# Kernel tuning notes

Hardware: AMD Instinct MI355X
Metric: run time of the kernel (lower is better)

## Reference

```python
import jax, jax.numpy as jnp
import numpy as np

BATCH, SEQ_LEN, ENC_IN = 64, 1536, 7
D_MODEL, N_HEADS, D_FF, E_LAYERS = 256, 8, 1024, 2
K_MA, FACTOR = 25, 1
EPS = 1e-5


def setup_inputs() -> dict:
    key = jax.random.key(0)
    ks = jax.random.split(key, 16)
    s = 0.02
    f32 = jnp.float32
    inp = {
        "x_enc": jax.random.normal(ks[0], (BATCH, SEQ_LEN, ENC_IN), f32),
        "emb_w": jax.random.normal(ks[1], (D_MODEL, ENC_IN, 3), f32) * s,
        "Wq": jax.random.normal(ks[2], (E_LAYERS, D_MODEL, D_MODEL), f32) * s,
        "bq": jnp.zeros((E_LAYERS, D_MODEL), f32),
        "Wk": jax.random.normal(ks[3], (E_LAYERS, D_MODEL, D_MODEL), f32) * s,
        "bk": jnp.zeros((E_LAYERS, D_MODEL), f32),
        "Wv": jax.random.normal(ks[4], (E_LAYERS, D_MODEL, D_MODEL), f32) * s,
        "bv": jnp.zeros((E_LAYERS, D_MODEL), f32),
        "Wo": jax.random.normal(ks[5], (E_LAYERS, D_MODEL, D_MODEL), f32) * s,
        "bo": jnp.zeros((E_LAYERS, D_MODEL), f32),
        "Wc1": jax.random.normal(ks[6], (E_LAYERS, D_FF, D_MODEL), f32) * s,
        "bc1": jnp.zeros((E_LAYERS, D_FF), f32),
        "Wc2": jax.random.normal(ks[7], (E_LAYERS, D_MODEL, D_FF), f32) * s,
        "bc2": jnp.zeros((E_LAYERS, D_MODEL), f32),
        "ln_w": jnp.ones((D_MODEL,), f32),
        "ln_b": jnp.zeros((D_MODEL,), f32),
        "proj_w": jax.random.normal(ks[8], (176, 2 * D_MODEL), f32) * s,
        "proj_b": jnp.zeros((176,), f32),
    }
    return inp


def _moving_avg(x, k):
    # x: [B,L,D]; replicate-pad (k-1)//2 both ends, mean filter size k (stride 1)
    p = (k - 1) // 2
    xp = jnp.concatenate([jnp.repeat(x[:, :1], p, axis=1), x,
                          jnp.repeat(x[:, -1:], p, axis=1)], axis=1)
    cs = jnp.cumsum(xp, axis=1)
    cs = jnp.concatenate([jnp.zeros_like(cs[:, :1]), cs], axis=1)
    return (cs[:, k:] - cs[:, :-k]) / k


def _decomp(x):
    mm = _moving_avg(x, K_MA)
    return x - mm, mm


def _autocorrelation(q, k, v):
    # q,k,v: [B,L,H,E] -> [B,L,H,E]
    B, L, H, E = q.shape
    qf = jnp.fft.rfft(jnp.transpose(q, (0, 2, 3, 1)), axis=-1)
    kf = jnp.fft.rfft(jnp.transpose(k, (0, 2, 3, 1)), axis=-1)
    corr = jnp.fft.irfft(qf * jnp.conj(kf), n=L, axis=-1)   # [B,H,E,L]
    vals = jnp.transpose(v, (0, 2, 3, 1))                    # [B,H,E,L]
    top_k = int(FACTOR * np.log(L))
    mean_corr = corr.mean(axis=(1, 2))                       # [B,L]
    weights, delay = jax.lax.top_k(mean_corr, top_k)         # [B,top_k]
    tmp_corr = jax.nn.softmax(weights, axis=-1)
    idx0 = jnp.arange(L)
    agg = jnp.zeros_like(vals)
    for i in range(top_k):                                    # small fixed count (7)
        idx = (idx0[None, :] + delay[:, i, None]) % L         # [B,L] circular delay
        pat = jnp.take_along_axis(vals, jnp.broadcast_to(idx[:, None, None, :], vals.shape), axis=-1)
        agg = agg + pat * tmp_corr[:, i, None, None, None]
    return jnp.transpose(agg, (0, 3, 1, 2))


def _attn_layer(x, Wq, bq, Wk, bk, Wv, bv, Wo, bo):
    B, L, _ = x.shape
    E = D_MODEL // N_HEADS
    q = (x @ Wq.T + bq).reshape(B, L, N_HEADS, E)
    k = (x @ Wk.T + bk).reshape(B, L, N_HEADS, E)
    v = (x @ Wv.T + bv).reshape(B, L, N_HEADS, E)
    out = _autocorrelation(q, k, v).reshape(B, L, D_MODEL)
    return out @ Wo.T + bo


def reference(x_enc, emb_w, Wq, bq, Wk, bk, Wv, bv, Wo, bo, Wc1, bc1, Wc2, bc2, ln_w, ln_b, proj_w, proj_b):
    # token embedding: circular-padded Conv1d(enc_in -> d_model, kernel 3, no bias)
    xp = jnp.concatenate([x_enc[:, -1:], x_enc, x_enc[:, :1]], axis=1)
    x = (jnp.einsum('blc,dc->bld', xp[:, :-2], emb_w[:, :, 0])
         + jnp.einsum('blc,dc->bld', xp[:, 1:-1], emb_w[:, :, 1])
         + jnp.einsum('blc,dc->bld', xp[:, 2:], emb_w[:, :, 2]))
    for l in range(E_LAYERS):
        a = _attn_layer(x, Wq[l], bq[l], Wk[l], bk[l], Wv[l], bv[l], Wo[l], bo[l])
        x, _ = _decomp(x + a)
        y = jax.nn.gelu(jnp.einsum('bld,fd->blf', x, Wc1[l]) + bc1[l], approximate=False)
        y = jnp.einsum('blf,df->bld', y, Wc2[l]) + bc2[l]
        x, _ = _decomp(x + y)
    # my_Layernorm: LN then subtract seq-mean
    mu = x.mean(-1, keepdims=True)
    var = ((x - mu) ** 2).mean(-1, keepdims=True)
    xh = (x - mu) / jnp.sqrt(var + EPS) * ln_w + ln_b
    x = xh - xh.mean(axis=1, keepdims=True)
    out = jnp.concatenate([x.mean(axis=1), x.max(axis=1)], axis=-1)  # [B, 2*d_model]
    out = jax.nn.gelu(out, approximate=False)
    return out @ proj_w.T + proj_b
```

## Files before the change

kernel.cpp:

```cpp
#include <hip/hip_runtime.h>
#include <math.h>

typedef _Float16 half_t;
typedef _Float16 half4 __attribute__((ext_vector_type(4)));
typedef _Float16 half8 __attribute__((ext_vector_type(8)));
typedef short short8 __attribute__((ext_vector_type(8)));
typedef float f32x4 __attribute__((ext_vector_type(4)));
typedef unsigned short u16;
typedef unsigned short u16x4 __attribute__((ext_vector_type(4)));

#define L_SEQ 1536

__device__ __forceinline__ u16 f2bf(float f){
  unsigned u = __float_as_uint(f);
  return (u16)((u + 0x7FFFu + ((u>>16)&1u)) >> 16);
}
__device__ __forceinline__ float bf2f(u16 h){ return __uint_as_float(((unsigned)h)<<16); }
__device__ __forceinline__ float gelu_f(float x){ return 0.5f*x*(1.f+erff(x*0.70710678118f)); }

__device__ __forceinline__ void load_lds16(const void* g, void* l){
  __builtin_amdgcn_global_load_lds((const __attribute__((address_space(1))) void*)g,
                                   (__attribute__((address_space(3))) void*)l, 16, 0, 0);
}
__device__ __forceinline__ f32x4 mfma_bf(short8 a, short8 b, f32x4 c){
  return __builtin_amdgcn_mfma_f32_16x16x32_bf16(a,b,c,0,0,0);
}
__device__ __forceinline__ f32x4 mfma_fp(half8 a, half8 b, f32x4 c){
  return __builtin_amdgcn_mfma_f32_16x16x32_f16(a,b,c,0,0,0);
}

__device__ __forceinline__ void store_pair(float v, size_t row, int d, u16* X2B){
  size_t r2 = row*512 + d;
  u16 hi = f2bf(v);
  X2B[r2] = hi;
  X2B[r2+256] = f2bf(v - bf2f(hi));
}

__global__ __launch_bounds__(256) void w4b_k(const float* __restrict__ W, u16* __restrict__ W4, int n){
  int i = blockIdx.x*256 + threadIdx.x;
  if (i >= n) return;
  int ro = i >> 8, c = i & 255;
  float v = W[i];
  u16 hi = f2bf(v);
  u16 lo = f2bf(v - bf2f(hi));
  u16* r = W4 + (size_t)ro*1024;
  r[c] = hi; r[c+256] = hi; r[c+512] = lo; r[c+768] = lo;
}
__global__ __launch_bounds__(256) void castb_k(const float* __restrict__ W, u16* __restrict__ Wb, int n){
  for (int i = blockIdx.x*256 + threadIdx.x; i < n; i += gridDim.x*256)
    Wb[i] = f2bf(W[i]);
}

__global__ __launch_bounds__(256) void embed_k(const float* __restrict__ XE, const float* __restrict__ EW,
                                               u16* __restrict__ X2B){
  __shared__ float xs[66*7];
  int b = blockIdx.x / 24, lc = blockIdx.x % 24;
  int l0 = lc*64;
  int tid = threadIdx.x;
  for (int i = tid; i < 66*7; i += 256){
    int r = i/7, c = i%7;
    int g = l0 - 1 + r; if (g < 0) g += L_SEQ; if (g >= L_SEQ) g -= L_SEQ;
    xs[i] = XE[((size_t)b*L_SEQ + g)*7 + c];
  }
  __syncthreads();
  int d = tid;
  float wp[21];
  #pragma unroll
  for (int i=0;i<21;i++) wp[i] = EW[d*21+i];
  for (int j = 0; j < 64; j++){
    float acc = 0.f;
    #pragma unroll
    for (int c = 0; c < 7; c++)
      #pragma unroll
      for (int k = 0; k < 3; k++) acc += xs[(j+k)*7+c] * wp[c*3+k];
    store_pair(acc, (size_t)b*L_SEQ + l0 + j, d, X2B);
  }
}

template<int EPI, bool KMOD>
__global__ __launch_bounds__(256) void gemm_k(const u16* __restrict__ A, int lda,
                                              const u16* __restrict__ B, int ldb,
                                              const float* __restrict__ bias,
                                              void* __restrict__ C, int ldc,
                                              const u16* __restrict__ res,
                                              int K){
  __shared__ __align__(16) u16 As[128*32];
  __shared__ __align__(16) u16 Bs[128*32];
  const int tid = threadIdx.x;
  const int wv = tid>>6, ln = tid&63;
  const int lrow = ln&15, lk = ln>>4;
  const int bm = blockIdx.x, bn = blockIdx.y;
  const int wr = wv>>1, wc = wv&1;
  f32x4 acc[4][4];
  #pragma unroll
  for (int i=0;i<4;i++)
    #pragma unroll
    for (int j=0;j<4;j++) acc[i][j] = f32x4{0.f,0.f,0.f,0.f};

  for (int k0 = 0; k0 < K; k0 += 32){
    int ka = KMOD ? (k0 & 511) : k0;
    #pragma unroll
    for (int p=0;p<2;p++){
      int chunk = (wv*2+p)*64 + ln;
      int row = chunk>>2, c16 = chunk&3;
      load_lds16(A + (size_t)(bm*128 + row)*lda + (ka + c16*8), &As[(size_t)chunk*8]);
      load_lds16(B + (size_t)(bn*128 + row)*ldb + (k0 + c16*8), &Bs[(size_t)chunk*8]);
    }
    __syncthreads();
    short8 av[4], bv[4];
    #pragma unroll
    for (int mi=0;mi<4;mi++) av[mi] = *(const short8*)&As[(wr*64 + mi*16 + lrow)*32 + lk*8];
    #pragma unroll
    for (int ni=0;ni<4;ni++) bv[ni] = *(const short8*)&Bs[(wc*64 + ni*16 + lrow)*32 + lk*8];
    #pragma unroll
    for (int mi=0;mi<4;mi++)
      #pragma unroll
      for (int ni=0;ni<4;ni++)
        acc[mi][ni] = mfma_bf(av[mi], bv[ni], acc[mi][ni]);
    __syncthreads();
  }

  #pragma unroll
  for (int mi=0;mi<4;mi++){
    #pragma unroll
    for (int ni=0;ni<4;ni++){
      int col = bn*128 + wc*64 + ni*16 + lrow;
      float bs = bias[col];
      #pragma unroll
      for (int r=0;r<4;r++){
        int row = bm*128 + wr*64 + mi*16 + lk*4 + r;
        float v = acc[mi][ni][r] + bs;
        if (EPI==0){ ((u16*)C)[(size_t)row*ldc + col] = f2bf(v); }
        else if (EPI==1){ ((u16*)C)[(size_t)row*ldc + col] = f2bf(gelu_f(v)); }
        else if (EPI==2){
          float rv = bf2f(res[(size_t)row*512 + col]) + bf2f(res[(size_t)row*512 + 256 + col]);
          ((float*)C)[(size_t)row*ldc + col] = v + rv;
        } else {
          half_t hi = (half_t)v;
          ((half_t*)C)[(size_t)row*512 + col] = hi;
          ((half_t*)C)[(size_t)row*512 + 256 + col] = (half_t)((v - (float)hi)*512.f);
        }
      }
    }
  }
}

__global__ __launch_bounds__(256) void gram_k(const u16* __restrict__ Q2, const u16* __restrict__ K2,
                                              float* __restrict__ MC){
  __shared__ __align__(16) union UN {
    struct { u16 As[256*32]; u16 Bs[64*32]; } s;
    float C[64][65];
  } u;
  const int tid = threadIdx.x, wv = tid>>6, ln = tid&63;
  const int lrow = ln&15, lk = ln>>4;
  int id = blockIdx.x;
  int low = id & 7, hi = id >> 3;
  int tb = hi & 7;
  int b  = ((hi >> 3) << 3) | low;
  const size_t base = (size_t)b*L_SEQ*512;
  f32x4 acc[4][4];
  #pragma unroll
  for (int i=0;i<4;i++)
    #pragma unroll
    for (int j=0;j<4;j++) acc[i][j] = f32x4{0.f,0.f,0.f,0.f};

  for (int jt = 0; jt < 24; jt++){
    int t0 = tb*192 + jt*64;
    for (int dt = 0; dt < 8; dt++){
      int d0 = dt*32;
      #pragma unroll
      for (int p=0;p<4;p++){
        int chunk = (p*4+wv)*64 + ln;
        int row = chunk>>2, c16 = chunk&3;
        int g = t0 + row; if (g >= L_SEQ) g -= L_SEQ;
        load_lds16(Q2 + base + (size_t)g*512 + d0 + c16*8, &u.s.As[(size_t)chunk*8]);
      }
      { int chunk = wv*64 + ln;
        int row = chunk>>2, c16 = chunk&3;
        load_lds16(K2 + base + (size_t)(jt*64+row)*512 + d0 + c16*8, &u.s.Bs[(size_t)chunk*8]); }
      __syncthreads();
      half8 av[4], bv[4];
      #pragma unroll
      for (int mi=0;mi<4;mi++) av[mi] = *(const half8*)&u.s.As[(wv*64 + mi*16 + lrow)*32 + lk*8];
      #pragma unroll
      for (int ni=0;ni<4;ni++) bv[ni] = *(const half8*)&u.s.Bs[(ni*16 + lrow)*32 + lk*8];
      #pragma unroll
      for (int mi=0;mi<4;mi++)
        #pragma unroll
        for (int ni=0;ni<4;ni++)
          acc[mi][ni] = mfma_fp(av[mi], bv[ni], acc[mi][ni]);
      __syncthreads();
    }
  }
  float dsum = 0.f;
  for (int r = 0; r < 4; r++){
    if (wv == r){
      #pragma unroll
      for (int mi=0;mi<4;mi++)
        #pragma unroll
        for (int ni=0;ni<4;ni++)
          #pragma unroll
          for (int rr=0;rr<4;rr++)
            u.C[mi*16 + lk*4 + rr][ni*16 + lrow] = acc[mi][ni][rr];
    }
    __syncthreads();
    if (tid < 192){
      int jlo = r*64 - tid;      if (jlo < 0) jlo = 0;
      int jhi = r*64 + 64 - tid; if (jhi > 64) jhi = 64;
      for (int j = jlo; j < jhi; j++) dsum += u.C[tid + j - r*64][j];
    }
    __syncthreads();
  }
  if (tid < 192) MC[(size_t)b*L_SEQ + tb*192 + tid] = dsum * (1.f/256.f);
}

__global__ __launch_bounds__(256) void topk_k(const float* __restrict__ MC, int* __restrict__ CANDI,
                                              int* __restrict__ NCAND){
  __shared__ float v[1536];
  __shared__ float rv[256]; __shared__ int ri[256];
  __shared__ float sred[256];
  __shared__ float s_margin;
  __shared__ float topv[16]; __shared__ int topi[16];
  int b = blockIdx.x, tid = threadIdx.x;
  const float* row = MC + (size_t)b*L_SEQ;
  float s = 0.f, ss = 0.f;
  for (int j=0;j<6;j++){ float x = row[tid+256*j]; v[tid+256*j] = x; s += x; ss += x*x; }
  sred[tid]=s; __syncthreads();
  for (int o=128;o>0;o>>=1){ if (tid<o) sred[tid]+=sred[tid+o]; __syncthreads(); }
  float mean = sred[0]*(1.f/1536.f); __syncthreads();
  sred[tid]=ss; __syncthreads();
  for (int o=128;o>0;o>>=1){ if (tid<o) sred[tid]+=sred[tid+o]; __syncthreads(); }
  if (tid==0){
    float var = sred[0]*(1.f/1536.f) - mean*mean; if (var < 0.f) var = 0.f;
    s_margin = 0.02f*sqrtf(var) + 1e-8f;
  }
  __syncthreads();
  for (int it = 0; it < 16; it++){
    float bv_ = -3.4e38f; int bi_ = 1<<30;
    for (int j=0;j<6;j++){ int idx = tid+256*j; float x = v[idx];
      if (x > bv_ || (x == bv_ && idx < bi_)){ bv_ = x; bi_ = idx; } }
    rv[tid]=bv_; ri[tid]=bi_; __syncthreads();
    for (int o=128;o>0;o>>=1){
      if (tid<o){
        float xo = rv[tid+o]; int io = ri[tid+o];
        if (xo > rv[tid] || (xo == rv[tid] && io < ri[tid])){ rv[tid]=xo; ri[tid]=io; }
      }
      __syncthreads();
    }
    if (tid==0){ topv[it]=rv[0]; topi[it]=ri[0]; v[ri[0]] = -3.4e38f; }
    __syncthreads();
  }
  if (tid==0){
    float thr = topv[6] - s_margin;
    int nc = 7; while (nc < 16 && topv[nc] >= thr) nc++;
    NCAND[b] = nc;
    for (int i=0;i<16;i++) CANDI[b*16+i] = topi[i];
  }
}

__global__ __launch_bounds__(256) void recompute3_k(const u16* __restrict__ Q2, const u16* __restrict__ K2,
                                                    const int* __restrict__ CANDI, const int* __restrict__ NCAND,
                                                    float* __restrict__ CANDV){
  int id = blockIdx.x;
  int low = id & 7, hi = id >> 3;
  int ci = hi & 15;
  int b = (hi >> 4)*8 + low;
  if (ci >= NCAND[b]) return;
  int tau = CANDI[b*16+ci];
  const half_t* qb = (const half_t*)Q2 + (size_t)b*L_SEQ*512;
  const half_t* kb = (const half_t*)K2 + (size_t)b*L_SEQ*512;
  int tid = threadIdx.x, wv = tid>>6, ln = tid&63;
  int d0 = ln*4;
  float acc = 0.f;
  #pragma unroll 4
  for (int t = wv; t < L_SEQ; t += 4){
    int g = t + tau; if (g >= L_SEQ) g -= L_SEQ;
    half4 qh = *(const half4*)(qb + (size_t)g*512 + d0);
    half4 ql = *(const half4*)(qb + (size_t)g*512 + 256 + d0);
    half4 kh = *(const half4*)(kb + (size_t)t*512 + d0);
    half4 kl = *(const half4*)(kb + (size_t)t*512 + 256 + d0);
    #pragma unroll
    for (int j=0;j<4;j++){
      float qv = (float)qh[j] + (float)ql[j]*(1.f/512.f);
      float kv = (float)kh[j] + (float)kl[j]*(1.f/512.f);
      acc += qv*kv;
    }
  }
  #pragma unroll
  for (int o=32;o>0;o>>=1) acc += __shfl_xor(acc,o);
  __shared__ float w4[4];
  if (ln==0) w4[wv]=acc;
  __syncthreads();
  if (tid==0) CANDV[b*16+ci] = (w4[0]+w4[1]+w4[2]+w4[3])*(1.f/256.f);
}

__global__ void select7_k(const int* __restrict__ CANDI, const float* __restrict__ CANDV,
                          const int* __restrict__ NCAND, int* __restrict__ DLY, float* __restrict__ WGT){
  int b = blockIdx.x;
  if (threadIdx.x != 0) return;
  int nc = NCAND[b];
  float vals[16]; int idx[16];
  #pragma unroll
  for (int i=0;i<16;i++){ vals[i] = (i<nc)? CANDV[b*16+i] : -3.4e38f; idx[i] = CANDI[b*16+i]; }
  for (int i=0;i<7;i++){
    int best=i;
    for (int j=i+1;j<16;j++)
      if (vals[j]>vals[best] || (vals[j]==vals[best] && idx[j]<idx[best])) best=j;
    float tv=vals[i]; vals[i]=vals[best]; vals[best]=tv;
    int ti=idx[i]; idx[i]=idx[best]; idx[best]=ti;
  }
  float m=vals[0], e[7], sum=0.f;
  #pragma unroll
  for (int i=0;i<7;i++){ e[i]=expf(vals[i]-m); sum+=e[i]; }
  #pragma unroll
  for (int i=0;i<7;i++){ WGT[b*8+i]=e[i]/sum; DLY[b*8+i]=idx[i]; }
}

__global__ __launch_bounds__(256) void agg_k(const u16* __restrict__ V, const int* __restrict__ DLY,
                                             const float* __restrict__ WGT, u16* __restrict__ AGG){
  int gid = blockIdx.x*256 + threadIdx.x;
  int b = gid / 49152;
  int rem = gid % 49152;
  int t = rem >> 5, du = rem & 31;
  float w[7]; int dl[7];
  #pragma unroll
  for (int i=0;i<7;i++){ w[i]=WGT[b*8+i]; dl[i]=DLY[b*8+i]; }
  float a[8] = {0,0,0,0,0,0,0,0};
  #pragma unroll
  for (int i=0;i<7;i++){
    int g = t + dl[i]; if (g >= L_SEQ) g -= L_SEQ;
    short8 hv = *(const short8*)(V + ((size_t)b*L_SEQ + g)*256 + du*8);
    #pragma unroll
    for (int j=0;j<8;j++) a[j] += w[i]*bf2f((u16)hv[j]);
  }
  short8 o;
  #pragma unroll
  for (int j=0;j<8;j++) o[j] = (short)f2bf(a[j]);
  *(short8*)(AGG + ((size_t)b*L_SEQ + t)*256 + du*8) = o;
}

__global__ __launch_bounds__(256) void decomp_k(const float* __restrict__ S, u16* __restrict__ X2B){
  int b = blockIdx.y, lc = blockIdx.x, d = threadIdx.x;
  const float* s = S + (size_t)b*L_SEQ*256;
  int l0 = lc*128;
  float w = 0.f;
  for (int j=-12;j<=12;j++){
    int g = l0+j; if (g < 0) g = 0; if (g > L_SEQ-1) g = L_SEQ-1;
    w += s[(size_t)g*256+d];
  }
  for (int l = l0; l < l0+128; l++){
    float c = s[(size_t)l*256+d];
    store_pair(c - w*(1.f/25.f), (size_t)b*L_SEQ + l, d, X2B);
    int ga = l+13; if (ga > L_SEQ-1) ga = L_SEQ-1;
    int gb = l-12; if (gb < 0) gb = 0;
    w += s[(size_t)ga*256+d] - s[(size_t)gb*256+d];
  }
}

__global__ __launch_bounds__(256) void ln_k(const u16* __restrict__ X2B, const float* __restrict__ LW,
                                            const float* __restrict__ LB, float* __restrict__ XH){
  int tid = threadIdx.x, wv = tid>>6, l_ = tid&63;
  f32x4 lw = *(const f32x4*)(LW + l_*4);
  f32x4 lb = *(const f32x4*)(LB + l_*4);
  size_t tok0 = (size_t)blockIdx.x*32 + wv*8;
  for (int it = 0; it < 8; it++){
    size_t tok = tok0 + it;
    const u16* xr = X2B + tok*512 + l_*4;
    u16x4 hi = *(const u16x4*)xr;
    u16x4 lo = *(const u16x4*)(xr+256);
    float v[4]; float s=0.f, ss=0.f;
    #pragma unroll
    for (int j=0;j<4;j++){ v[j] = bf2f(hi[j]) + bf2f(lo[j]); s += v[j]; ss += v[j]*v[j]; }
    #pragma unroll
    for (int o=32;o>0;o>>=1){ s += __shfl_xor(s,o); ss += __shfl_xor(ss,o); }
    float mean = s*(1.f/256.f);
    float var = ss*(1.f/256.f) - mean*mean;
    float rstd = rsqrtf(var + 1e-5f);
    #pragma unroll
    for (int j=0;j<4;j++)
      XH[tok*256 + l_*4 + j] = (v[j]-mean)*rstd*lw[j] + lb[j];
  }
}

__global__ __launch_bounds__(256) void colred_k(const float* __restrict__ XH, float* __restrict__ RS,
                                                float* __restrict__ RM){
  int b = blockIdx.y, lc = blockIdx.x, d = threadIdx.x;
  float s = 0.f, m = -3.4e38f;
  for (int l = lc*128; l < lc*128+128; l++){
    float x = XH[(size_t)(b*L_SEQ + l)*256 + d];
    s += x; m = fmaxf(m, x);
  }
  RS[((size_t)b*12+lc)*256+d] = s;
  RM[((size_t)b*12+lc)*256+d] = m;
}

__global__ __launch_bounds__(256) void final_k(const float* __restrict__ RS, const float* __restrict__ RM,
                                               const float* __restrict__ PW, const float* __restrict__ PB,
                                               float* __restrict__ OUT){
  __shared__ float feat[256];
  int b = blockIdx.x, tid = threadIdx.x;
  float s = 0.f, m = -3.4e38f;
  for (int c=0;c<12;c++){
    s += RS[((size_t)b*12+c)*256+tid];
    m = fmaxf(m, RM[((size_t)b*12+c)*256+tid]);
  }
  float mu = s*(1.f/1536.f);
  feat[tid] = gelu_f(m - mu);
  __syncthreads();
  if (tid < 176){
    float acc = PB[tid];
    for (int d=0; d<256; d++) acc += feat[d]*PW[(size_t)tid*512 + 256 + d];
    OUT[(size_t)b*176 + tid] = acc;
  }
}

extern "C" void kernel_launch(void* const* d_in, const int* in_sizes, int n_in,
                              void* d_out, int out_size, void* d_ws, size_t ws_size,
                              hipStream_t stream){
  const float* x_enc=(const float*)d_in[0];
  const float* emb_w=(const float*)d_in[1];
  const float* Wq=(const float*)d_in[2];  const float* bq=(const float*)d_in[3];
  const float* Wk=(const float*)d_in[4];  const float* bk=(const float*)d_in[5];
  const float* Wv=(const float*)d_in[6];  const float* bv=(const float*)d_in[7];
  const float* Wo=(const float*)d_in[8];  const float* bo=(const float*)d_in[9];
  const float* Wc1=(const float*)d_in[10]; const float* bc1=(const float*)d_in[11];
  const float* Wc2=(const float*)d_in[12]; const float* bc2=(const float*)d_in[13];
  const float* ln_w=(const float*)d_in[14]; const float* ln_b=(const float*)d_in[15];
  const float* pw=(const float*)d_in[16];  const float* pb=(const float*)d_in[17];
  (void)in_sizes; (void)n_in; (void)out_size;

  int G = 1;
  while (G < 8){
    size_t need = (size_t)32*1024*1024 + 3ull*(size_t)(98304/G)*1024ull;
    if (need <= ws_size) break;
    G *= 2;
  }
  const int NBG = 64 / G;
  const int NT  = NBG * L_SEQ;

  char* ws = (char*)d_ws;
  size_t off = 0;
  auto alloc = [&](size_t bytes)->void*{
    void* p = ws + off; off += (bytes + 255) & ~(size_t)255; return p;
  };
  u16* W4Q  = (u16*)alloc((size_t)2*256*1024*2);
  u16* W4K  = (u16*)alloc((size_t)2*256*1024*2);
  u16* WVb  = (u16*)alloc((size_t)2*256*256*2);
  u16* WOb  = (u16*)alloc((size_t)2*256*256*2);
  u16* WC1b = (u16*)alloc((size_t)2*1024*256*2);
  u16* WC2b = (u16*)alloc((size_t)2*256*1024*2);
  float* MC = (float*)alloc((size_t)64*L_SEQ*4);
  int*  CANDI=(int*)  alloc(64*16*4);
  float*CANDV=(float*)alloc(64*16*4);
  int*  NCAND=(int*)  alloc(64*4);
  int*  DLY = (int*)  alloc(64*8*4);
  float*WGT = (float*)alloc(64*8*4);
  float*RS  = (float*)alloc((size_t)64*12*256*4);
  float*RM  = (float*)alloc((size_t)64*12*256*4);
  u16* X2B = (u16*)alloc((size_t)NT*512*2);
  u16* Q2  = (u16*)alloc((size_t)NT*512*2);
  u16* K2  = (u16*)alloc((size_t)NT*512*2);

  float* SUM = (float*)K2;
  u16*   VH  = Q2;
  u16*   AGG = Q2 + (size_t)NT*256;
  u16*   HH  = Q2;
  float* XHF = (float*)Q2;

  w4b_k<<<512,256,0,stream>>>(Wq, W4Q, 2*256*256);
  w4b_k<<<512,256,0,stream>>>(Wk, W4K, 2*256*256);
  castb_k<<<512,256,0,stream>>>(Wv, WVb, 2*256*256);
  castb_k<<<512,256,0,stream>>>(Wo, WOb, 2*256*256);
  castb_k<<<2048,256,0,stream>>>(Wc1, WC1b, 2*1024*256);
  castb_k<<<2048,256,0,stream>>>(Wc2, WC2b, 2*256*1024);

  for (int g = 0; g < G; g++){
    const float* xe = x_enc + (size_t)g*NBG*L_SEQ*7;
    float* outg = (float*)d_out + (size_t)g*NBG*176;

    embed_k<<<NT/64,256,0,stream>>>(xe, emb_w, X2B);

    for (int l = 0; l < 2; l++){
      gemm_k<3,true><<<dim3(NT/128,2),256,0,stream>>>(X2B,512, W4Q+(size_t)l*262144,1024, bq+l*256, Q2, 512, nullptr, 1024);
      gemm_k<3,true><<<dim3(NT/128,2),256,0,stream>>>(X2B,512, W4K+(size_t)l*262144,1024, bk+l*256, K2, 512, nullptr, 1024);
      gram_k<<<NBG*8,256,0,stream>>>(Q2, K2, MC);
      topk_k<<<NBG,256,0,stream>>>(MC, CANDI, NCAND);
      recompute3_k<<<NBG*16,256,0,stream>>>(Q2, K2, CANDI, NCAND, CANDV);
      select7_k<<<NBG,64,0,stream>>>(CANDI, CANDV, NCAND, DLY, WGT);
      gemm_k<0,false><<<dim3(NT/128,2),256,0,stream>>>(X2B,512, WVb+(size_t)l*65536,256, bv+l*256, VH, 256, nullptr, 256);
      agg_k<<<NT/8,256,0,stream>>>(VH, DLY, WGT, AGG);
      gemm_k<2,false><<<dim3(NT/128,2),256,0,stream>>>(AGG,256, WOb+(size_t)l*65536,256, bo+l*256, SUM, 256, X2B, 256);
      decomp_k<<<dim3(12,NBG),256,0,stream>>>(SUM, X2B);
      for (int c = 0; c < 4; c++){
        const u16* Ac = X2B + (size_t)c*(NT/4)*512;
        gemm_k<1,false><<<dim3(NT/512,8),256,0,stream>>>(Ac,512, WC1b+(size_t)l*262144,256, bc1+l*1024, HH, 1024, nullptr, 256);
        gemm_k<2,false><<<dim3(NT/512,2),256,0,stream>>>(HH,1024, WC2b+(size_t)l*262144,1024, bc2+l*256,
                                                         SUM+(size_t)c*(NT/4)*256, 256, X2B+(size_t)c*(NT/4)*512, 1024);
      }
      decomp_k<<<dim3(12,NBG),256,0,stream>>>(SUM, X2B);
    }

    ln_k<<<NT/32,256,0,stream>>>(X2B, ln_w, ln_b, XHF);
    colred_k<<<dim3(12,NBG),256,0,stream>>>(XHF, RS, RM);
    final_k<<<NBG,256,0,stream>>>(RS, RM, pw, pb, outg);
  }
}
```

Measured before the change: 2.752 ms.

## Double-buffer LDS tiles with XOR swizzle in GEMM and gram kernels

Both the generic bf16 GEMM and the fp16 gram kernel now keep two LDS tile buffers and issue the next K-tile's global-to-LDS loads before computing on the current one. This removes one barrier per iteration and overlaps memory latency with MFMA work. The 16-byte column chunks are XOR-swizzled by row on store and on read to reduce LDS bank conflicts. The FFN is also split into 2 chunks instead of 4, which means fewer and larger launches. That split needs a larger HH scratch buffer, and doubling the LDS per block may lower occupancy.

```diff
diff --git a/kernel.cpp b/kernel.cpp
--- a/kernel.cpp
+++ b/kernel.cpp
@@ -84,8 +84,8 @@
                                               void* __restrict__ C, int ldc,
                                               const u16* __restrict__ res,
                                               int K){
-  __shared__ __align__(16) u16 As[128*32];
-  __shared__ __align__(16) u16 Bs[128*32];
+  __shared__ __align__(16) u16 As[2][128*32];
+  __shared__ __align__(16) u16 Bs[2][128*32];
   const int tid = threadIdx.x;
   const int wv = tid>>6, ln = tid&63;
   const int lrow = ln&15, lk = ln>>4;
@@ -97,27 +97,37 @@
     #pragma unroll
     for (int j=0;j<4;j++) acc[i][j] = f32x4{0.f,0.f,0.f,0.f};
 
-  for (int k0 = 0; k0 < K; k0 += 32){
+  const int nt = K >> 5;
+  auto stage = [&](int buf, int t){
+    int k0 = t*32;
     int ka = KMOD ? (k0 & 511) : k0;
     #pragma unroll
     for (int p=0;p<2;p++){
       int chunk = (wv*2+p)*64 + ln;
       int row = chunk>>2, c16 = chunk&3;
-      load_lds16(A + (size_t)(bm*128 + row)*lda + (ka + c16*8), &As[(size_t)chunk*8]);
-      load_lds16(B + (size_t)(bn*128 + row)*ldb + (k0 + c16*8), &Bs[(size_t)chunk*8]);
-    }
+      int sw = (row>>1)&3;
+      load_lds16(A + (size_t)(bm*128 + row)*lda + (ka + ((c16^sw)*8)), &As[buf][(size_t)chunk*8]);
+      load_lds16(B + (size_t)(bn*128 + row)*ldb + (k0 + ((c16^sw)*8)), &Bs[buf][(size_t)chunk*8]);
+    }
+  };
+
+  stage(0, 0);
+  int cur = 0;
+  const int swR = (lrow>>1)&3;
+  for (int t = 0; t < nt; t++){
     __syncthreads();
+    if (t+1 < nt) stage(cur^1, t+1);
     short8 av[4], bv[4];
     #pragma unroll
-    for (int mi=0;mi<4;mi++) av[mi] = *(const short8*)&As[(wr*64 + mi*16 + lrow)*32 + lk*8];
-    #pragma unroll
-    for (int ni=0;ni<4;ni++) bv[ni] = *(const short8*)&Bs[(wc*64 + ni*16 + lrow)*32 + lk*8];
+    for (int mi=0;mi<4;mi++) av[mi] = *(const short8*)&As[cur][(wr*64 + mi*16 + lrow)*32 + ((lk^swR)*8)];
+    #pragma unroll
+    for (int ni=0;ni<4;ni++) bv[ni] = *(const short8*)&Bs[cur][(wc*64 + ni*16 + lrow)*32 + ((lk^swR)*8)];
     #pragma unroll
     for (int mi=0;mi<4;mi++)
       #pragma unroll
       for (int ni=0;ni<4;ni++)
         acc[mi][ni] = mfma_bf(av[mi], bv[ni], acc[mi][ni]);
-    __syncthreads();
+    cur ^= 1;
   }
 
   #pragma unroll
@@ -148,7 +158,7 @@
 __global__ __launch_bounds__(256) void gram_k(const u16* __restrict__ Q2, const u16* __restrict__ K2,
                                               float* __restrict__ MC){
   __shared__ __align__(16) union UN {
-    struct { u16 As[256*32]; u16 Bs[64*32]; } s;
+    struct { u16 As[2][256*32]; u16 Bs[2][64*32]; } s;
     float C[64][65];
   } u;
   const int tid = threadIdx.x, wv = tid>>6, ln = tid&63;
@@ -164,34 +174,43 @@
     #pragma unroll
     for (int j=0;j<4;j++) acc[i][j] = f32x4{0.f,0.f,0.f,0.f};
 
-  for (int jt = 0; jt < 24; jt++){
-    int t0 = tb*192 + jt*64;
-    for (int dt = 0; dt < 8; dt++){
-      int d0 = dt*32;
+  auto stageG = [&](int buf, int it){
+    int jt = it>>3, dt = it&7;
+    int t0 = tb*192 + jt*64, d0 = dt*32;
+    #pragma unroll
+    for (int p=0;p<4;p++){
+      int chunk = (p*4+wv)*64 + ln;
+      int row = chunk>>2, c16 = chunk&3;
+      int sw = (row>>1)&3;
+      int g = t0 + row; if (g >= L_SEQ) g -= L_SEQ;
+      load_lds16(Q2 + base + (size_t)g*512 + d0 + ((c16^sw)*8), &u.s.As[buf][(size_t)chunk*8]);
+    }
+    { int chunk = wv*64 + ln;
+      int row = chunk>>2, c16 = chunk&3;
+      int sw = (row>>1)&3;
+      load_lds16(K2 + base + (size_t)(jt*64+row)*512 + d0 + ((c16^sw)*8), &u.s.Bs[buf][(size_t)chunk*8]); }
+  };
+
+  stageG(0, 0);
+  int cur = 0;
+  const int swR = (lrow>>1)&3;
+  for (int it = 0; it < 192; it++){
+    __syncthreads();
+    if (it+1 < 192) stageG(cur^1, it+1);
+    half8 av[4], bv[4];
+    #pragma unroll
+    for (int mi=0;mi<4;mi++) av[mi] = *(const half8*)&u.s.As[cur][(wv*64 + mi*16 + lrow)*32 + ((lk^swR)*8)];
+    #pragma unroll
+    for (int ni=0;ni<4;ni++) bv[ni] = *(const half8*)&u.s.Bs[cur][(ni*16 + lrow)*32 + ((lk^swR)*8)];
+    #pragma unroll
+    for (int mi=0;mi<4;mi++)
       #pragma unroll
-      for (int p=0;p<4;p++){
-        int chunk = (p*4+wv)*64 + ln;
-        int row = chunk>>2, c16 = chunk&3;
-        int g = t0 + row; if (g >= L_SEQ) g -= L_SEQ;
-        load_lds16(Q2 + base + (size_t)g*512 + d0 + c16*8, &u.s.As[(size_t)chunk*8]);
-      }
-      { int chunk = wv*64 + ln;
-        int row = chunk>>2, c16 = chunk&3;
-        load_lds16(K2 + base + (size_t)(jt*64+row)*512 + d0 + c16*8, &u.s.Bs[(size_t)chunk*8]); }
-      __syncthreads();
-      half8 av[4], bv[4];
-      #pragma unroll
-      for (int mi=0;mi<4;mi++) av[mi] = *(const half8*)&u.s.As[(wv*64 + mi*16 + lrow)*32 + lk*8];
-      #pragma unroll
-      for (int ni=0;ni<4;ni++) bv[ni] = *(const half8*)&u.s.Bs[(ni*16 + lrow)*32 + lk*8];
-      #pragma unroll
-      for (int mi=0;mi<4;mi++)
-        #pragma unroll
-        for (int ni=0;ni<4;ni++)
-          acc[mi][ni] = mfma_fp(av[mi], bv[ni], acc[mi][ni]);
-      __syncthreads();
-    }
-  }
+      for (int ni=0;ni<4;ni++)
+        acc[mi][ni] = mfma_fp(av[mi], bv[ni], acc[mi][ni]);
+    cur ^= 1;
+  }
+  __syncthreads();
+
   float dsum = 0.f;
   for (int r = 0; r < 4; r++){
     if (wv == r){
@@ -491,11 +510,11 @@
       agg_k<<<NT/8,256,0,stream>>>(VH, DLY, WGT, AGG);
       gemm_k<2,false><<<dim3(NT/128,2),256,0,stream>>>(AGG,256, WOb+(size_t)l*65536,256, bo+l*256, SUM, 256, X2B, 256);
       decomp_k<<<dim3(12,NBG),256,0,stream>>>(SUM, X2B);
-      for (int c = 0; c < 4; c++){
-        const u16* Ac = X2B + (size_t)c*(NT/4)*512;
-        gemm_k<1,false><<<dim3(NT/512,8),256,0,stream>>>(Ac,512, WC1b+(size_t)l*262144,256, bc1+l*1024, HH, 1024, nullptr, 256);
-        gemm_k<2,false><<<dim3(NT/512,2),256,0,stream>>>(HH,1024, WC2b+(size_t)l*262144,1024, bc2+l*256,
-                                                         SUM+(size_t)c*(NT/4)*256, 256, X2B+(size_t)c*(NT/4)*512, 1024);
+      for (int c = 0; c < 2; c++){
+        const u16* Ac = X2B + (size_t)c*(NT/2)*512;
+        gemm_k<1,false><<<dim3(NT/256,8),256,0,stream>>>(Ac,512, WC1b+(size_t)l*262144,256, bc1+l*1024, HH, 1024, nullptr, 256);
+        gemm_k<2,false><<<dim3(NT/256,2),256,0,stream>>>(HH,1024, WC2b+(size_t)l*262144,1024, bc2+l*256,
+                                                         SUM+(size_t)c*(NT/2)*256, 256, X2B+(size_t)c*(NT/2)*512, 1024);
       }
       decomp_k<<<dim3(12,NBG),256,0,stream>>>(SUM, X2B);
     }
```

Measured after the change: 2.389 ms. 1.15x faster.
